# Performance work log

Hardware: AMD Instinct MI355X
Metric: run time of the kernel (lower is better)

Reference implementation:

```python
import jax, jax.numpy as jnp
import numpy as np

N, D, P, Q = 4096, 512, 8, 32
MARGIN = 1.0
L2_WEIGHT = 0.005
EPS = 1e-6  # torch.nn.PairwiseDistance default eps, added to the difference


def setup_inputs() -> dict:
    key = jax.random.key(0)
    k1, k2, k3 = jax.random.split(key, 3)
    batch = jax.random.normal(k1, (N, D), dtype=jnp.float32)
    anchors = jnp.arange(N, dtype=jnp.int64) if jax.config.jax_enable_x64 else jnp.arange(N, dtype=jnp.int32)
    pos_idx = jax.random.randint(k2, (N, P), 0, N)
    neg_idx = jax.random.randint(k3, (N, Q), 0, N)
    return {"batch": batch, "anchors": anchors, "pos_idx": pos_idx, "neg_idx": neg_idx}


def reference(batch, anchors, pos_idx, neg_idx):
    # batch: [N, D]; anchors: [N]; pos_idx: [N, P]; neg_idx: [N, Q]
    a = batch[anchors]                       # [N, D]
    # PairwiseDistance(p=2): (sum |x - y + eps|^2)^(1/2)
    d_pos = jnp.sqrt(jnp.sum((a[:, None, :] - batch[pos_idx] + EPS) ** 2, axis=-1))  # [N, P]
    d_neg = jnp.sqrt(jnp.sum((a[:, None, :] - batch[neg_idx] + EPS) ** 2, axis=-1))  # [N, Q]
    pos_term = jax.scipy.special.logsumexp(d_pos, axis=1)            # [N]
    neg_term = jax.scipy.special.logsumexp(MARGIN - d_neg, axis=1)   # [N]
    per_anchor = jax.nn.relu(pos_term + neg_term)                    # [N]
    l2_term = L2_WEIGHT * jnp.mean(jnp.sqrt(jnp.sum(batch ** 2, axis=1)))
    return jnp.mean(per_anchor) + l2_term
```

## Files before the change

kernel.cpp:

```cpp
#include <hip/hip_runtime.h>
#include <math.h>
#include <float.h>

#define NN 4096
#define DD 512
#define PP 8
#define QQ 32
#define NB_TOT (PP + QQ)
#define PER_WAVE (NB_TOT / 4)
constexpr float MARGIN = 1.0f;
constexpr float L2W    = 0.005f;
constexpr float EPS    = 1e-6f;

__device__ inline float wave_reduce_sum(float v) {
    v += __shfl_xor(v, 32, 64);
    v += __shfl_xor(v, 16, 64);
    v += __shfl_xor(v,  8, 64);
    v += __shfl_xor(v,  4, 64);
    v += __shfl_xor(v,  2, 64);
    v += __shfl_xor(v,  1, 64);
    return v;
}

__device__ inline float wave_reduce_max(float v) {
    v = fmaxf(v, __shfl_xor(v, 32, 64));
    v = fmaxf(v, __shfl_xor(v, 16, 64));
    v = fmaxf(v, __shfl_xor(v,  8, 64));
    v = fmaxf(v, __shfl_xor(v,  4, 64));
    v = fmaxf(v, __shfl_xor(v,  2, 64));
    v = fmaxf(v, __shfl_xor(v,  1, 64));
    return v;
}

__global__ __launch_bounds__(256) void dist_kernel(
    const float* __restrict__ batch,
    const int*   __restrict__ anchors,
    const int*   __restrict__ pos_idx,
    const int*   __restrict__ neg_idx,
    float*       __restrict__ ws)
{
    const int i    = blockIdx.x;
    const int tid  = threadIdx.x;
    const int lane = tid & 63;
    const int wave = tid >> 6;

    __shared__ float dist[NB_TOT];
    __shared__ float norm_sh;

    const int arow = anchors[i];
    const float* __restrict__ ap = batch + (size_t)arow * DD + lane * 8;
    const float4 a0 = *reinterpret_cast<const float4*>(ap);
    const float4 a1 = *reinterpret_cast<const float4*>(ap + 4);

    if (wave == 3) {
        const float* __restrict__ rp = batch + (size_t)i * DD + lane * 8;
        const float4 r0 = *reinterpret_cast<const float4*>(rp);
        const float4 r1 = *reinterpret_cast<const float4*>(rp + 4);
        float s = r0.x*r0.x + r0.y*r0.y + r0.z*r0.z + r0.w*r0.w
                + r1.x*r1.x + r1.y*r1.y + r1.z*r1.z + r1.w*r1.w;
        s = wave_reduce_sum(s);
        if (lane == 0) norm_sh = sqrtf(s);
    }

    int idxs[PER_WAVE];
    #pragma unroll
    for (int t = 0; t < PER_WAVE; ++t) {
        const int j = wave * PER_WAVE + t;
        idxs[t] = (j < PP) ? pos_idx[i * PP + j] : neg_idx[i * QQ + (j - PP)];
    }

    float4 b0[PER_WAVE], b1[PER_WAVE];
    #pragma unroll
    for (int t = 0; t < PER_WAVE; ++t) {
        const float* __restrict__ bp = batch + (size_t)idxs[t] * DD + lane * 8;
        b0[t] = *reinterpret_cast<const float4*>(bp);
        b1[t] = *reinterpret_cast<const float4*>(bp + 4);
    }

    float s[PER_WAVE];
    #pragma unroll
    for (int t = 0; t < PER_WAVE; ++t) {
        float d, acc = 0.0f;
        d = a0.x - b0[t].x + EPS; acc += d * d;
        d = a0.y - b0[t].y + EPS; acc += d * d;
        d = a0.z - b0[t].z + EPS; acc += d * d;
        d = a0.w - b0[t].w + EPS; acc += d * d;
        d = a1.x - b1[t].x + EPS; acc += d * d;
        d = a1.y - b1[t].y + EPS; acc += d * d;
        d = a1.z - b1[t].z + EPS; acc += d * d;
        d = a1.w - b1[t].w + EPS; acc += d * d;
        s[t] = acc;
    }

    #pragma unroll
    for (int t = 0; t < PER_WAVE; ++t) s[t] = wave_reduce_sum(s[t]);

    if (lane == 0) {
        #pragma unroll
        for (int t = 0; t < PER_WAVE; ++t)
            dist[wave * PER_WAVE + t] = sqrtf(s[t]);
    }

    __syncthreads();

    if (wave == 0) {
        const float d = (lane < NB_TOT) ? dist[lane] : 0.0f;

        const bool pact = (lane < PP);
        const float pm = wave_reduce_max(pact ? d : -FLT_MAX);
        const float ps = wave_reduce_sum(pact ? expf(d - pm) : 0.0f);
        const float pos_term = pm + logf(ps);

        const bool nact = (lane >= PP) && (lane < NB_TOT);
        const float nv = MARGIN - d;
        const float nm = wave_reduce_max(nact ? nv : -FLT_MAX);
        const float ns = wave_reduce_sum(nact ? expf(nv - nm) : 0.0f);
        const float neg_term = nm + logf(ns);

        if (lane == 0)
            ws[i] = fmaxf(0.0f, pos_term + neg_term) + L2W * norm_sh;
    }
}

__global__ __launch_bounds__(256) void reduce_kernel(
    const float* __restrict__ ws, float* __restrict__ out)
{
    const int tid  = threadIdx.x;
    const int lane = tid & 63;
    const int wave = tid >> 6;

    const float4* __restrict__ w4 = reinterpret_cast<const float4*>(ws);
    float s = 0.0f;
    #pragma unroll
    for (int k = 0; k < 4; ++k) {
        const float4 v = w4[tid + 256 * k];
        s += v.x + v.y + v.z + v.w;
    }
    s = wave_reduce_sum(s);

    __shared__ float part[4];
    if (lane == 0) part[wave] = s;
    __syncthreads();
    if (tid == 0)
        out[0] = (part[0] + part[1] + part[2] + part[3]) * (1.0f / (float)NN);
}

extern "C" void kernel_launch(void* const* d_in, const int* in_sizes, int n_in,
                              void* d_out, int out_size, void* d_ws, size_t ws_size,
                              hipStream_t stream) {
    const float* batch   = (const float*)d_in[0];
    const int*   anchors = (const int*)d_in[1];
    const int*   pos_idx = (const int*)d_in[2];
    const int*   neg_idx = (const int*)d_in[3];
    float*       ws      = (float*)d_ws;
    float*       out     = (float*)d_out;

    dist_kernel<<<NN, 256, 0, stream>>>(batch, anchors, pos_idx, neg_idx, ws);
    reduce_kernel<<<1, 256, 0, stream>>>(ws, out);
}
```

Before: 91.74 us.

## Assign each neighbor row to an 8-lane group across five waves

Restructures the distance kernel so that each 8-lane group handles one neighbor row across the full 512-wide vector. Five waves now cover all 40 neighbors, replacing the previous scheme where each wave iterated over 10 neighbors with full-wave reductions. The anchor row is loaded per lane with EPS pre-added, and each group needs only a 3-step shuffle reduction instead of ten 6-step full-wave reductions. In exchange, each lane holds 32 float4 values in registers, and each 8-lane group reads 2KB rows in 128-byte strided chunks, which may lower occupancy and change coalescing.

```diff
diff --git a/kernel.cpp b/kernel.cpp
--- a/kernel.cpp
+++ b/kernel.cpp
@@ -7,7 +7,7 @@
 #define PP 8
 #define QQ 32
 #define NB_TOT (PP + QQ)
-#define PER_WAVE (NB_TOT / 4)
+#define NWAVES 5
 constexpr float MARGIN = 1.0f;
 constexpr float L2W    = 0.005f;
 constexpr float EPS    = 1e-6f;
@@ -32,7 +32,14 @@
     return v;
 }
 
-__global__ __launch_bounds__(256) void dist_kernel(
+__device__ inline float group8_reduce_sum(float v) {
+    v += __shfl_xor(v, 1, 64);
+    v += __shfl_xor(v, 2, 64);
+    v += __shfl_xor(v, 4, 64);
+    return v;
+}
+
+__global__ __launch_bounds__(320) void dist_kernel(
     const float* __restrict__ batch,
     const int*   __restrict__ anchors,
     const int*   __restrict__ pos_idx,
@@ -43,16 +50,24 @@
     const int tid  = threadIdx.x;
     const int lane = tid & 63;
     const int wave = tid >> 6;
+    const int g    = lane >> 3;
+    const int k    = lane & 7;
 
     __shared__ float dist[NB_TOT];
     __shared__ float norm_sh;
 
     const int arow = anchors[i];
-    const float* __restrict__ ap = batch + (size_t)arow * DD + lane * 8;
-    const float4 a0 = *reinterpret_cast<const float4*>(ap);
-    const float4 a1 = *reinterpret_cast<const float4*>(ap + 4);
+    const float* __restrict__ ap = batch + (size_t)arow * DD + k * 4;
+    float4 a[16];
+    #pragma unroll
+    for (int c = 0; c < 16; ++c)
+        a[c] = *reinterpret_cast<const float4*>(ap + c * 32);
+    #pragma unroll
+    for (int c = 0; c < 16; ++c) {
+        a[c].x += EPS; a[c].y += EPS; a[c].z += EPS; a[c].w += EPS;
+    }
 
-    if (wave == 3) {
+    if (wave == 0) {
         const float* __restrict__ rp = batch + (size_t)i * DD + lane * 8;
         const float4 r0 = *reinterpret_cast<const float4*>(rp);
         const float4 r1 = *reinterpret_cast<const float4*>(rp + 4);
@@ -62,44 +77,28 @@
         if (lane == 0) norm_sh = sqrtf(s);
     }
 
-    int idxs[PER_WAVE];
+    const int j    = wave * 8 + g;
+    const int nidx = (j < PP) ? pos_idx[i * PP + j]
+                              : neg_idx[i * QQ + (j - PP)];
+
+    const float* __restrict__ bp = batch + (size_t)nidx * DD + k * 4;
+    float4 b[16];
     #pragma unroll
-    for (int t = 0; t < PER_WAVE; ++t) {
-        const int j = wave * PER_WAVE + t;
-        idxs[t] = (j < PP) ? pos_idx[i * PP + j] : neg_idx[i * QQ + (j - PP)];
+    for (int c = 0; c < 16; ++c)
+        b[c] = *reinterpret_cast<const float4*>(bp + c * 32);
+
+    float acc = 0.0f;
+    #pragma unroll
+    for (int c = 0; c < 16; ++c) {
+        float d;
+        d = a[c].x - b[c].x; acc = fmaf(d, d, acc);
+        d = a[c].y - b[c].y; acc = fmaf(d, d, acc);
+        d = a[c].z - b[c].z; acc = fmaf(d, d, acc);
+        d = a[c].w - b[c].w; acc = fmaf(d, d, acc);
     }
 
-    float4 b0[PER_WAVE], b1[PER_WAVE];
-    #pragma unroll
-    for (int t = 0; t < PER_WAVE; ++t) {
-        const float* __restrict__ bp = batch + (size_t)idxs[t] * DD + lane * 8;
-        b0[t] = *reinterpret_cast<const float4*>(bp);
-        b1[t] = *reinterpret_cast<const float4*>(bp + 4);
-    }
-
-    float s[PER_WAVE];
-    #pragma unroll
-    for (int t = 0; t < PER_WAVE; ++t) {
-        float d, acc = 0.0f;
-        d = a0.x - b0[t].x + EPS; acc += d * d;
-        d = a0.y - b0[t].y + EPS; acc += d * d;
-        d = a0.z - b0[t].z + EPS; acc += d * d;
-        d = a0.w - b0[t].w + EPS; acc += d * d;
-        d = a1.x - b1[t].x + EPS; acc += d * d;
-        d = a1.y - b1[t].y + EPS; acc += d * d;
-        d = a1.z - b1[t].z + EPS; acc += d * d;
-        d = a1.w - b1[t].w + EPS; acc += d * d;
-        s[t] = acc;
-    }
-
-    #pragma unroll
-    for (int t = 0; t < PER_WAVE; ++t) s[t] = wave_reduce_sum(s[t]);
-
-    if (lane == 0) {
-        #pragma unroll
-        for (int t = 0; t < PER_WAVE; ++t)
-            dist[wave * PER_WAVE + t] = sqrtf(s[t]);
-    }
+    acc = group8_reduce_sum(acc);
+    if (k == 0) dist[j] = sqrtf(acc);
 
     __syncthreads();
 
@@ -155,6 +154,6 @@
     float*       ws      = (float*)d_ws;
     float*       out     = (float*)d_out;
 
-    dist_kernel<<<NN, 256, 0, stream>>>(batch, anchors, pos_idx, neg_idx, ws);
+    dist_kernel<<<NN, 320, 0, stream>>>(batch, anchors, pos_idx, neg_idx, ws);
     reduce_kernel<<<1, 256, 0, stream>>>(ws, out);
 }
```

After: 100.4 us. 1.09x slower.

## Split each anchor across two blocks and move logsumexp into a separate reduction kernel

Applied to the files above, without the earlier changes.

The distance kernel now launches two blocks per anchor, each wave handling five neighbours, and writes raw distances and row norms to workspace instead of doing the logsumexp in-block after a barrier. A new reduction kernel with 64 blocks computes the logsumexp terms per anchor and atomically accumulates into the output, which a separate init kernel zeroes first. EPS is folded into the anchor once and the squared sums use fmaf. This is meant to raise parallelism and occupancy and remove the block-wide sync, at the cost of an extra launch, workspace traffic and a non-deterministic atomic sum.

```diff
diff --git a/kernel.cpp b/kernel.cpp
--- a/kernel.cpp
+++ b/kernel.cpp
@@ -6,8 +6,8 @@
 #define DD 512
 #define PP 8
 #define QQ 32
-#define NB_TOT (PP + QQ)
-#define PER_WAVE (NB_TOT / 4)
+#define NB_TOT 40
+#define NPW 5
 constexpr float MARGIN = 1.0f;
 constexpr float L2W    = 0.005f;
 constexpr float EPS    = 1e-6f;
@@ -32,79 +32,99 @@
     return v;
 }
 
-__global__ __launch_bounds__(256) void dist_kernel(
+__global__ void init_out_kernel(float* out) {
+    if (threadIdx.x == 0) out[0] = 0.0f;
+}
+
+__global__ __launch_bounds__(256, 7) void dist_kernel(
     const float* __restrict__ batch,
     const int*   __restrict__ anchors,
     const int*   __restrict__ pos_idx,
     const int*   __restrict__ neg_idx,
-    float*       __restrict__ ws)
+    float*       __restrict__ dists,
+    float*       __restrict__ norms)
 {
-    const int i    = blockIdx.x;
+    const int b    = blockIdx.x;
+    const int i    = b >> 1;
+    const int h    = b & 1;
     const int tid  = threadIdx.x;
     const int lane = tid & 63;
     const int wave = tid >> 6;
-
-    __shared__ float dist[NB_TOT];
-    __shared__ float norm_sh;
+    const int jb   = h * 20 + wave * NPW;
 
     const int arow = anchors[i];
     const float* __restrict__ ap = batch + (size_t)arow * DD + lane * 8;
-    const float4 a0 = *reinterpret_cast<const float4*>(ap);
-    const float4 a1 = *reinterpret_cast<const float4*>(ap + 4);
+    float4 a0 = *reinterpret_cast<const float4*>(ap);
+    float4 a1 = *reinterpret_cast<const float4*>(ap + 4);
+    a0.x += EPS; a0.y += EPS; a0.z += EPS; a0.w += EPS;
+    a1.x += EPS; a1.y += EPS; a1.z += EPS; a1.w += EPS;
 
-    if (wave == 3) {
+    if (h == 0 && wave == 0) {
         const float* __restrict__ rp = batch + (size_t)i * DD + lane * 8;
         const float4 r0 = *reinterpret_cast<const float4*>(rp);
         const float4 r1 = *reinterpret_cast<const float4*>(rp + 4);
         float s = r0.x*r0.x + r0.y*r0.y + r0.z*r0.z + r0.w*r0.w
                 + r1.x*r1.x + r1.y*r1.y + r1.z*r1.z + r1.w*r1.w;
         s = wave_reduce_sum(s);
-        if (lane == 0) norm_sh = sqrtf(s);
+        if (lane == 0) norms[i] = sqrtf(s);
     }
 
-    int idxs[PER_WAVE];
+    int idxs[NPW];
     #pragma unroll
-    for (int t = 0; t < PER_WAVE; ++t) {
-        const int j = wave * PER_WAVE + t;
+    for (int t = 0; t < NPW; ++t) {
+        const int j = jb + t;
         idxs[t] = (j < PP) ? pos_idx[i * PP + j] : neg_idx[i * QQ + (j - PP)];
     }
 
-    float4 b0[PER_WAVE], b1[PER_WAVE];
+    float4 b0[NPW], b1[NPW];
     #pragma unroll
-    for (int t = 0; t < PER_WAVE; ++t) {
+    for (int t = 0; t < NPW; ++t) {
         const float* __restrict__ bp = batch + (size_t)idxs[t] * DD + lane * 8;
         b0[t] = *reinterpret_cast<const float4*>(bp);
         b1[t] = *reinterpret_cast<const float4*>(bp + 4);
     }
 
-    float s[PER_WAVE];
+    float s[NPW];
     #pragma unroll
-    for (int t = 0; t < PER_WAVE; ++t) {
+    for (int t = 0; t < NPW; ++t) {
         float d, acc = 0.0f;
-        d = a0.x - b0[t].x + EPS; acc += d * d;
-        d = a0.y - b0[t].y + EPS; acc += d * d;
-        d = a0.z - b0[t].z + EPS; acc += d * d;
-        d = a0.w - b0[t].w + EPS; acc += d * d;
-        d = a1.x - b1[t].x + EPS; acc += d * d;
-        d = a1.y - b1[t].y + EPS; acc += d * d;
-        d = a1.z - b1[t].z + EPS; acc += d * d;
-        d = a1.w - b1[t].w + EPS; acc += d * d;
+        d = a0.x - b0[t].x; acc = fmaf(d, d, acc);
+        d = a0.y - b0[t].y; acc = fmaf(d, d, acc);
+        d = a0.z - b0[t].z; acc = fmaf(d, d, acc);
+        d = a0.w - b0[t].w; acc = fmaf(d, d, acc);
+        d = a1.x - b1[t].x; acc = fmaf(d, d, acc);
+        d = a1.y - b1[t].y; acc = fmaf(d, d, acc);
+        d = a1.z - b1[t].z; acc = fmaf(d, d, acc);
+        d = a1.w - b1[t].w; acc = fmaf(d, d, acc);
         s[t] = acc;
     }
 
     #pragma unroll
-    for (int t = 0; t < PER_WAVE; ++t) s[t] = wave_reduce_sum(s[t]);
+    for (int t = 0; t < NPW; ++t) s[t] = wave_reduce_sum(s[t]);
 
-    if (lane == 0) {
-        #pragma unroll
-        for (int t = 0; t < PER_WAVE; ++t)
-            dist[wave * PER_WAVE + t] = sqrtf(s[t]);
-    }
+    float v = s[0];
+    v = (lane == 1) ? s[1] : v;
+    v = (lane == 2) ? s[2] : v;
+    v = (lane == 3) ? s[3] : v;
+    v = (lane == 4) ? s[4] : v;
+    if (lane < NPW) dists[i * NB_TOT + jb + lane] = sqrtf(v);
+}
 
-    __syncthreads();
+__global__ __launch_bounds__(256) void lse_reduce_kernel(
+    const float* __restrict__ dists,
+    const float* __restrict__ norms,
+    float*       __restrict__ out)
+{
+    const int tid  = threadIdx.x;
+    const int lane = tid & 63;
+    const int wave = tid >> 6;
 
-    if (wave == 0) {
-        const float d = (lane < NB_TOT) ? dist[lane] : 0.0f;
+    float accum = 0.0f;
+    const int abase = (blockIdx.x * 4 + wave) * 16;
+
+    for (int u = 0; u < 16; ++u) {
+        const int a = abase + u;
+        const float d = (lane < NB_TOT) ? dists[a * NB_TOT + lane] : 0.0f;
 
         const bool pact = (lane < PP);
         const float pm = wave_reduce_max(pact ? d : -FLT_MAX);
@@ -118,31 +138,14 @@
         const float neg_term = nm + logf(ns);
 
         if (lane == 0)
-            ws[i] = fmaxf(0.0f, pos_term + neg_term) + L2W * norm_sh;
+            accum += fmaxf(0.0f, pos_term + neg_term) + L2W * norms[a];
     }
-}
-
-__global__ __launch_bounds__(256) void reduce_kernel(
-    const float* __restrict__ ws, float* __restrict__ out)
-{
-    const int tid  = threadIdx.x;
-    const int lane = tid & 63;
-    const int wave = tid >> 6;
-
-    const float4* __restrict__ w4 = reinterpret_cast<const float4*>(ws);
-    float s = 0.0f;
-    #pragma unroll
-    for (int k = 0; k < 4; ++k) {
-        const float4 v = w4[tid + 256 * k];
-        s += v.x + v.y + v.z + v.w;
-    }
-    s = wave_reduce_sum(s);
 
     __shared__ float part[4];
-    if (lane == 0) part[wave] = s;
+    if (lane == 0) part[wave] = accum;
     __syncthreads();
     if (tid == 0)
-        out[0] = (part[0] + part[1] + part[2] + part[3]) * (1.0f / (float)NN);
+        atomicAdd(out, (part[0] + part[1] + part[2] + part[3]) * (1.0f / (float)NN));
 }
 
 extern "C" void kernel_launch(void* const* d_in, const int* in_sizes, int n_in,
@@ -152,9 +155,11 @@
     const int*   anchors = (const int*)d_in[1];
     const int*   pos_idx = (const int*)d_in[2];
     const int*   neg_idx = (const int*)d_in[3];
-    float*       ws      = (float*)d_ws;
+    float*       dists   = (float*)d_ws;
+    float*       norms   = (float*)d_ws + NN * NB_TOT;
     float*       out     = (float*)d_out;
 
-    dist_kernel<<<NN, 256, 0, stream>>>(batch, anchors, pos_idx, neg_idx, ws);
-    reduce_kernel<<<1, 256, 0, stream>>>(ws, out);
+    init_out_kernel<<<1, 1, 0, stream>>>(out);
+    dist_kernel<<<2 * NN, 256, 0, stream>>>(batch, anchors, pos_idx, neg_idx, dists, norms);
+    lse_reduce_kernel<<<64, 256, 0, stream>>>(dists, norms, out);
 }
```

Result: slower. 108.8 us (+18.6%).
